# Optimization experiments

Hardware: AMD Instinct MI355X
Metric: run time of the kernel (lower is better)

## Reference

```python
import jax, jax.numpy as jnp
import numpy as np

NHEAD = 8
NEG_INF = -1e9
LN_EPS = 1e-5


def setup_inputs() -> dict:
    key = jax.random.key(0)
    ks = jax.random.split(key, 8)
    B, Q, N, C = 2, 256, 16384, 256
    return {
        "queries": jax.random.normal(ks[0], (B, Q, C), jnp.float32),
        "vid_features": jax.random.normal(ks[1], (B, C, N), jnp.float32),
        "vid_mask": jax.random.uniform(ks[2], (B, Q, N), jnp.float32),
        "pos_embed": jax.random.normal(ks[3], (B, C, N), jnp.float32),
        "query_embed": jax.random.normal(ks[4], (B, Q, C), jnp.float32),
        "in_proj_w": jax.random.normal(ks[5], (3 * C, C), jnp.float32) * 0.02,
        "in_proj_b": jnp.zeros((3 * C,), jnp.float32),
        "out_proj_w": jax.random.normal(ks[6], (C, C), jnp.float32) * 0.02,
        "out_proj_b": jnp.zeros((C,), jnp.float32),
        "ln_gamma": jnp.ones((C,), jnp.float32),
        "ln_beta": jnp.zeros((C,), jnp.float32),
    }


def reference(queries, vid_features, vid_mask, pos_embed, query_embed,
              in_proj_w, in_proj_b, out_proj_w, out_proj_b, ln_gamma, ln_beta):
    B, Q, C = queries.shape
    H = NHEAD
    d = C // H

    vf = jnp.transpose(vid_features, (0, 2, 1))   # B N C
    pe = jnp.transpose(pos_embed, (0, 2, 1))      # B N C

    q_in = queries + query_embed                  # with_pos_embed on queries
    k_in = vf + pe                                # with_pos_embed on keys
    v_in = vf

    wq, wk, wv = jnp.split(in_proj_w, 3, axis=0)
    bq, bk, bv = jnp.split(in_proj_b, 3)

    q = (q_in @ wq.T + bq).reshape(B, Q, H, d)
    k = (k_in @ wk.T + bk).reshape(B, -1, H, d)
    v = (v_in @ wv.T + bv).reshape(B, -1, H, d)

    scale = 1.0 / jnp.sqrt(jnp.asarray(d, q.dtype))
    logits = jnp.einsum('bqhd,bnhd->bhqn', q, k) * scale  # B H Q N

    # Hard masking: block keys where mask prob < 0.5; if a query row is
    # fully blocked, fall back to unmasked attention (avoid NaN softmax).
    blocked = vid_mask < 0.5                                 # B Q N
    all_blocked = jnp.all(blocked, axis=-1, keepdims=True)   # B Q 1
    blocked = blocked & jnp.logical_not(all_blocked)
    logits = jnp.where(blocked[:, None, :, :], NEG_INF, logits)

    attn = jax.nn.softmax(logits, axis=-1)
    ctx = jnp.einsum('bhqn,bnhd->bqhd', attn, v).reshape(B, Q, C)
    tgt2 = ctx @ out_proj_w.T + out_proj_b

    # residual + LayerNorm (dropout p=0.0 -> identity)
    x = queries + tgt2
    mu = jnp.mean(x, axis=-1, keepdims=True)
    var = jnp.mean(jnp.square(x - mu), axis=-1, keepdims=True)
    return (x - mu) / jnp.sqrt(var + LN_EPS) * ln_gamma + ln_beta
```

## Files before the change

kernel.cpp:

```cpp
#include <hip/hip_runtime.h>
#include <stdint.h>

#define B_ 2
#define Q_ 256
#define N_ 16384
#define C_ 256
#define H_ 8
#define D_ 32
#define NC_ 32
#define SCALE 0.17677669529663687f

typedef __bf16 bf16x8 __attribute__((ext_vector_type(8)));
typedef float f32x4 __attribute__((ext_vector_type(4)));

__device__ __forceinline__ uint16_t f2bf(float f) {
  union { float f; uint32_t u; } c; c.f = f;
  uint32_t r = c.u + 0x7FFFu + ((c.u >> 16) & 1u);
  return (uint16_t)(r >> 16);
}
__device__ __forceinline__ float bf2f(uint16_t u) {
  union { uint32_t u; float f; } c; c.u = (uint32_t)u << 16;
  return c.f;
}
__device__ __forceinline__ uint32_t pk2(float a, float b) {
  return (uint32_t)f2bf(a) | ((uint32_t)f2bf(b) << 16);
}
__device__ __forceinline__ void lgkm0_barrier() {
  __builtin_amdgcn_sched_barrier(0);
  asm volatile("s_waitcnt lgkmcnt(0)" ::: "memory");
  __builtin_amdgcn_sched_barrier(0);
  __builtin_amdgcn_s_barrier();
  __builtin_amdgcn_sched_barrier(0);
}

__global__ __launch_bounds__(256) void prep(const float* __restrict__ inw,
                                            const float* __restrict__ outw,
                                            const float* __restrict__ vm,
                                            uint16_t* __restrict__ wb,
                                            float* __restrict__ woT,
                                            uint32_t* __restrict__ mb) {
  __shared__ __align__(16) char sh[4352];
  const int bid = blockIdx.x;
  const int t = threadIdx.x;
  if (bid < 96) {
    const int i = (bid * 256 + t) * 8;
    const float4 a = *reinterpret_cast<const float4*>(inw + i);
    const float4 b = *reinterpret_cast<const float4*>(inw + i + 4);
    ushort4 lo = {f2bf(a.x), f2bf(a.y), f2bf(a.z), f2bf(a.w)};
    ushort4 hi = {f2bf(b.x), f2bf(b.y), f2bf(b.z), f2bf(b.w)};
    *reinterpret_cast<ushort4*>(wb + i) = lo;
    *reinterpret_cast<ushort4*>(wb + i + 4) = hi;
  } else if (bid < 160) {
    float(*s)[33] = reinterpret_cast<float(*)[33]>(sh);
    const int bb = bid - 96;
    const int bx = bb & 7, by = bb >> 3;
    const int r0 = by * 32, c0 = bx * 32;
    const int tr = t >> 5, tc = t & 31;
#pragma unroll
    for (int k = 0; k < 4; ++k)
      s[tr + 8 * k][tc] = outw[(size_t)(r0 + tr + 8 * k) * 256 + c0 + tc];
    __syncthreads();
#pragma unroll
    for (int k = 0; k < 4; ++k)
      woT[(size_t)(c0 + tr + 8 * k) * 256 + r0 + tc] = s[tc][tr + 8 * k];
  } else {
    uint8_t(*nib)[256] = reinterpret_cast<uint8_t(*)[256]>(sh);
    __shared__ int wcnt[4];
    __shared__ int tot;
    const int bq = bid - 160;
    const float* row = vm + (size_t)bq * N_;
    const int lane = t & 63;
    int cnt = 0;
#pragma unroll
    for (int i = 0; i < 16; ++i) {
      const float4 v = *reinterpret_cast<const float4*>(&row[i * 1024 + 4 * t]);
      const uint32_t nb = (v.x < 0.5f ? 1u : 0u) | (v.y < 0.5f ? 2u : 0u) |
                          (v.z < 0.5f ? 4u : 0u) | (v.w < 0.5f ? 8u : 0u);
      nib[i][t] = (uint8_t)nb;
      cnt += __popc(nb);
    }
    for (int o = 32; o > 0; o >>= 1) cnt += __shfl_down(cnt, o, 64);
    if (lane == 0) wcnt[t >> 6] = cnt;
    __syncthreads();
    if (t == 0) tot = wcnt[0] + wcnt[1] + wcnt[2] + wcnt[3];
    __syncthreads();
    const bool allb = (tot == N_);
    uint32_t* dst = mb + (size_t)bq * 512;
#pragma unroll
    for (int k = 0; k < 2; ++k) {
      const int w = k * 256 + t;
      const int i = w >> 5, tw = w & 31;
      const uint2 u = *reinterpret_cast<const uint2*>(&nib[i][8 * tw]);
      uint32_t y0 = u.x & 0x0F0F0F0Fu; y0 = y0 | (y0 >> 4);
      uint32_t y1 = u.y & 0x0F0F0F0Fu; y1 = y1 | (y1 >> 4);
      const uint32_t word = (y0 & 0xFFu) | (((y0 >> 16) & 0xFFu) << 8) |
                            ((y1 & 0xFFu) << 16) | (((y1 >> 16) & 0xFFu) << 24);
      dst[w] = allb ? 0u : word;
    }
  }
}

__global__ __launch_bounds__(512, 2) void kvqproj(const float* __restrict__ vf,
                                                  const float* __restrict__ pe,
                                                  const float* __restrict__ queries,
                                                  const float* __restrict__ qembed,
                                                  const uint16_t* __restrict__ wkv,
                                                  const float* __restrict__ bias,
                                                  uint16_t* __restrict__ Kh,
                                                  uint16_t* __restrict__ Vh,
                                                  uint16_t* __restrict__ Qb) {
  __shared__ __align__(16) uint16_t shpool[8][64][40];
  const int bid = blockIdx.x;
  const int t = threadIdx.x, wid = t >> 6, lane = t & 63;
  const int g = lane >> 4, c15 = lane & 15;

  if (bid >= 8) {
    const int kb = bid - 8;
    const bool isK = kb < 512;
    const int u = isK ? kb : kb - 512;
    const int b = u >> 8, nt = u & 255;
    const int n0 = nt * 64;
    const int wc = wid;

    const uint16_t* Wsec = wkv + (size_t)((isK ? 256 : 512) + wc * 32 + c15) * C_;

    f32x4 acc[8];
    if (isK) {
#pragma unroll
      for (int cf = 0; cf < 2; ++cf) {
        f32x4 iv;
#pragma unroll
        for (int j = 0; j < 4; ++j) iv[j] = bias[256 + wc * 32 + cf * 16 + 4 * g + j];
#pragma unroll
        for (int nf = 0; nf < 4; ++nf) acc[cf * 4 + nf] = iv;
      }
    } else {
#pragma unroll
      for (int cf = 0; cf < 2; ++cf) {
        const float bv = bias[512 + wc * 32 + cf * 16 + c15];
        const f32x4 iv = {bv, bv, bv, bv};
#pragma unroll
        for (int nf = 0; nf < 4; ++nf) acc[nf * 2 + cf] = iv;
      }
    }

    const int cq = t >> 5, q2 = t & 31;
    const float* Xb = vf + ((size_t)b * C_ + 2 * cq) * N_ + n0 + 2 * q2;
    const float* Pb = pe + ((size_t)b * C_ + 2 * cq) * N_ + n0 + 2 * q2;
    const int cqs = cq ^ (((q2 >> 2) & 3) << 2);

    float2 xA0, xA1, pA0, pA1, xB0, xB1, pB0, pB1;
    bf16x8 Wa[2], Wz[2];

#define LOADW(W, s)                                                          \
    {                                                                        \
      _Pragma("unroll") for (int cf = 0; cf < 2; ++cf)                       \
          W[cf] = *(const bf16x8*)(Wsec + (size_t)cf * 16 * C_ + (s) * 32 + g * 8); \
    }
#define LOADA(X0, X1, P0, P1, s)                                             \
    {                                                                        \
      const float* x_ = Xb + (size_t)(s) * 32 * N_;                          \
      X0 = *(const float2*)x_;                                               \
      X1 = *(const float2*)(x_ + N_);                                        \
      if (isK) {                                                             \
        const float* p_ = Pb + (size_t)(s) * 32 * N_;                        \
        P0 = *(const float2*)p_;                                             \
        P1 = *(const float2*)(p_ + N_);                                      \
      }                                                                      \
    }
#define WRITEA(X0, X1, P0, P1, buf)                                          \
    {                                                                        \
      uint32_t w0_, w1_;                                                     \
      if (isK) {                                                             \
        w0_ = pk2(X0.x + P0.x, X1.x + P1.x);                                 \
        w1_ = pk2(X0.y + P0.y, X1.y + P1.y);                                 \
      } else {                                                               \
        w0_ = pk2(X0.x, X1.x);                                               \
        w1_ = pk2(X0.y, X1.y);                                               \
      }                                                                      \
      *(uint32_t*)&shpool[buf][2 * q2][2 * cqs] = w0_;                       \
      *(uint32_t*)&shpool[buf][2 * q2 + 1][2 * cqs] = w1_;                   \
    }
#define COMPUTE(buf, W)                                                      \
    {                                                                        \
      _Pragma("unroll") for (int nf = 0; nf < 4; ++nf) {                     \
        const int r_ = nf * 16 + c15;                                        \
        const bf16x8 F_ = *(const bf16x8*)&shpool[buf][r_][(g ^ ((r_ >> 3) & 3)) * 8]; \
        if (isK) {                                                           \
          _Pragma("unroll") for (int cf = 0; cf < 2; ++cf)                   \
              acc[cf * 4 + nf] = __builtin_amdgcn_mfma_f32_16x16x32_bf16(    \
                  W[cf], F_, acc[cf * 4 + nf], 0, 0, 0);                     \
        } else {                                                             \
          _Pragma("unroll") for (int cf = 0; cf < 2; ++cf)                   \
              acc[nf * 2 + cf] = __builtin_amdgcn_mfma_f32_16x16x32_bf16(    \
                  F_, W[cf], acc[nf * 2 + cf], 0, 0, 0);                     \
        }                                                                    \
      }                                                                      \
    }

    LOADW(Wa, 0);
    LOADA(xA0, xA1, pA0, pA1, 0);
    LOADA(xB0, xB1, pB0, pB1, 1);
    LOADW(Wz, 1); WRITEA(xA0, xA1, pA0, pA1, 0); LOADA(xA0, xA1, pA0, pA1, 2);
    lgkm0_barrier(); COMPUTE(0, Wa); __builtin_amdgcn_sched_barrier(0);
    LOADW(Wa, 2); WRITEA(xB0, xB1, pB0, pB1, 1); LOADA(xB0, xB1, pB0, pB1, 3);
    lgkm0_barrier(); COMPUTE(1, Wz); __builtin_amdgcn_sched_barrier(0);
    LOADW(Wz, 3); WRITEA(xA0, xA1, pA0, pA1, 0); LOADA(xA0, xA1, pA0, pA1, 4);
    lgkm0_barrier(); COMPUTE(0, Wa); __builtin_amdgcn_sched_barrier(0);
    LOADW(Wa, 4); WRITEA(xB0, xB1, pB0, pB1, 1); LOADA(xB0, xB1, pB0, pB1, 5);
    lgkm0_barrier(); COMPUTE(1, Wz); __builtin_amdgcn_sched_barrier(0);
    LOADW(Wz, 5); WRITEA(xA0, xA1, pA0, pA1, 0); LOADA(xA0, xA1, pA0, pA1, 6);
    lgkm0_barrier(); COMPUTE(0, Wa); __builtin_amdgcn_sched_barrier(0);
    LOADW(Wa, 6); WRITEA(xB0, xB1, pB0, pB1, 1); LOADA(xB0, xB1, pB0, pB1, 7);
    lgkm0_barrier(); COMPUTE(1, Wz); __builtin_amdgcn_sched_barrier(0);
    LOADW(Wz, 7); WRITEA(xA0, xA1, pA0, pA1, 0);
    lgkm0_barrier(); COMPUTE(0, Wa); __builtin_amdgcn_sched_barrier(0);
    WRITEA(xB0, xB1, pB0, pB1, 1);
    lgkm0_barrier(); COMPUTE(1, Wz); __builtin_amdgcn_sched_barrier(0);

#undef LOADW
#undef LOADA
#undef WRITEA
#undef COMPUTE

    if (isK) {
      uint16_t* Kp = Kh + (size_t)(b * H_ + wc) * N_ * D_;
#pragma unroll
      for (int cf = 0; cf < 2; ++cf)
#pragma unroll
        for (int nf = 0; nf < 4; ++nf) {
          const f32x4 a = acc[cf * 4 + nf];
          uint2 pkv;
          pkv.x = pk2(a[0], a[1]);
          pkv.y = pk2(a[2], a[3]);
          *(uint2*)&Kp[(size_t)(n0 + nf * 16 + c15) * D_ + cf * 16 + 4 * g] = pkv;
        }
    } else {
      uint16_t* Vp = Vh + (size_t)(b * H_ + wc) * D_ * N_;
#pragma unroll
      for (int nf = 0; nf < 4; ++nf)
#pragma unroll
        for (int cf = 0; cf < 2; ++cf) {
          const f32x4 a = acc[nf * 2 + cf];
          uint2 pkv;
          pkv.x = pk2(a[0], a[1]);
          pkv.y = pk2(a[2], a[3]);
          *(uint2*)&Vp[(size_t)(cf * 16 + c15) * N_ + n0 + nf * 16 + 4 * g] = pkv;
        }
    }
  } else {
    const int qb = bid;
    const int q0g = qb * 64;
    const int b = q0g >> 8, q0 = q0g & 255;
    const int r = t >> 3, c0 = (t & 7) * 32, s = t & 7;
    const float* Qrow = queries + (size_t)(q0g + r) * C_ + c0;
    const float* Erow = qembed + (size_t)(q0g + r) * C_ + c0;
#pragma unroll
    for (int ph = 0; ph < 2; ++ph) {
      float4 a4[4], e4[4];
#pragma unroll
      for (int k = 0; k < 4; ++k) a4[k] = reinterpret_cast<const float4*>(Qrow + ph * 16)[k];
#pragma unroll
      for (int k = 0; k < 4; ++k) e4[k] = reinterpret_cast<const float4*>(Erow + ph * 16)[k];
      const float* af = reinterpret_cast<const float*>(a4);
      const float* ef = reinterpret_cast<const float*>(e4);
#pragma unroll
      for (int i = 0; i < 16; ++i) {
        const int cl = ph * 16 + i;
        const int col = cl ^ (8 * ((r >> 3) & 3));
        shpool[s][r][col] = f2bf(af[i] + ef[i]);
      }
      __builtin_amdgcn_sched_barrier(0);
    }
    lgkm0_barrier();

    const int w = wid;
    f32x4 acc[4][2];
#pragma unroll
    for (int nf = 0; nf < 2; ++nf) {
      const float bv = bias[w * 32 + nf * 16 + c15];
      const f32x4 iv = {bv, bv, bv, bv};
#pragma unroll
      for (int qf = 0; qf < 4; ++qf) acc[qf][nf] = iv;
    }
#pragma unroll
    for (int s8 = 0; s8 < 8; ++s8) {
      bf16x8 Bf[2];
#pragma unroll
      for (int nf = 0; nf < 2; ++nf)
        Bf[nf] = *reinterpret_cast<const bf16x8*>(
            wkv + (size_t)(w * 32 + nf * 16 + c15) * C_ + s8 * 32 + g * 8);
#pragma unroll
      for (int qf = 0; qf < 4; ++qf) {
        const int rr = qf * 16 + c15;
        const bf16x8 Af = *reinterpret_cast<const bf16x8*>(
            &shpool[s8][rr][8 * (g ^ ((rr >> 3) & 3))]);
#pragma unroll
        for (int nf = 0; nf < 2; ++nf)
          acc[qf][nf] = __builtin_amdgcn_mfma_f32_16x16x32_bf16(Af, Bf[nf], acc[qf][nf], 0, 0, 0);
      }
    }
#pragma unroll
    for (int qf = 0; qf < 4; ++qf)
#pragma unroll
      for (int nf = 0; nf < 2; ++nf)
#pragma unroll
        for (int j = 0; j < 4; ++j) {
          const int q = q0 + qf * 16 + 4 * g + j;
          const int dk = nf * 16 + c15;
          Qb[((size_t)(b * H_ + w) * Q_ + q) * D_ + dk] = f2bf(acc[qf][nf][j] * SCALE);
        }
  }
}

__global__ __launch_bounds__(512) void attn(const uint16_t* __restrict__ Qb,
                                            const uint16_t* __restrict__ Kh,
                                            const uint16_t* __restrict__ Vh,
                                            const uint32_t* __restrict__ mb,
                                            uint16_t* __restrict__ ctx_part,
                                            float* __restrict__ lsum_part) {
  const int bid = blockIdx.x;
  const int nc = bid & 31, h = (bid >> 5) & 7, b = bid >> 8;
  const int t = threadIdx.x, wid = t >> 6, lane = t & 63;
  const int g = lane >> 4, c15 = lane & 15;
  const int qw0 = wid * 32;
  const int nbase = nc * (N_ / NC_);
  constexpr int SS = (N_ / NC_) / 128;

  __shared__ __align__(16) uint16_t kst[2][128][40];
  __shared__ __align__(16) uint16_t vst[2][32][136];
  __shared__ __align__(16) uint16_t plds[8][32][40];

  const uint16_t* Qp = Qb + (size_t)(b * H_ + h) * Q_ * D_;
  bf16x8 qfr[2];
#pragma unroll
  for (int qf = 0; qf < 2; ++qf)
    qfr[qf] = *reinterpret_cast<const bf16x8*>(Qp + (size_t)(qw0 + qf * 16 + c15) * D_ + g * 8);

  f32x4 acc[2][2];
  const f32x4 zero4 = {0.f, 0.f, 0.f, 0.f};
#pragma unroll
  for (int qf = 0; qf < 2; ++qf)
#pragma unroll
    for (int dvf = 0; dvf < 2; ++dvf) acc[qf][dvf] = zero4;
  float lsum[2][4] = {};

  const uint32_t* mrow = mb + (size_t)b * Q_ * (N_ / 32);

  const int krow = t >> 2, kch = t & 3;
  const uint16_t* ksrc = Kh + ((size_t)(b * H_ + h) * N_ + nbase + krow) * 32 + kch * 8;
  const int vrow = t >> 4, vch = t & 15;
  const uint16_t* vsrc = Vh + ((size_t)(b * H_ + h) * 32 + vrow) * N_ + nbase + vch * 8;

  uint4 kreg = *(const uint4*)ksrc;
  uint4 vreg = *(const uint4*)vsrc;

  int cur = 0;
  for (int ss = 0; ss < SS; ++ss) {
    *(uint4*)&kst[cur][krow][kch * 8] = kreg;
    *(uint4*)&vst[cur][vrow][vch * 8] = vreg;
    if (ss < SS - 1) {
      kreg = *(const uint4*)(ksrc + (size_t)(ss + 1) * 128 * 32);
      vreg = *(const uint4*)(vsrc + (ss + 1) * 128);
    }
    lgkm0_barrier();

    const int nstart = nbase + ss * 128;
#pragma unroll
    for (int half = 0; half < 2; ++half) {
      uint32_t mw[2][4][2];
#pragma unroll
      for (int qf = 0; qf < 2; ++qf)
#pragma unroll
        for (int j = 0; j < 4; ++j) {
          const int q = qw0 + qf * 16 + 4 * g + j;
          const uint2 u = *reinterpret_cast<const uint2*>(
              &mrow[(size_t)q * (N_ / 32) + (nstart >> 5) + half * 2]);
          mw[qf][j][0] = u.x;
          mw[qf][j][1] = u.y;
        }
#pragma unroll
      for (int s2 = 0; s2 < 2; ++s2) {
        const int sub = half * 2 + s2;
        const int nl0 = sub * 32;
        bf16x8 kfr[2];
#pragma unroll
        for (int nf = 0; nf < 2; ++nf)
          kfr[nf] = *reinterpret_cast<const bf16x8*>(&kst[cur][nl0 + nf * 16 + c15][g * 8]);
        f32x4 s[2][2];
#pragma unroll
        for (int qf = 0; qf < 2; ++qf)
#pragma unroll
          for (int nf = 0; nf < 2; ++nf)
            s[qf][nf] = __builtin_amdgcn_mfma_f32_16x16x32_bf16(qfr[qf], kfr[nf], zero4, 0, 0, 0);

#pragma unroll
        for (int qf = 0; qf < 2; ++qf) {
#pragma unroll
          for (int j = 0; j < 4; ++j) {
            const uint32_t wmask = mw[qf][j][s2];
#pragma unroll
            for (int nf = 0; nf < 2; ++nf) {
              const int bit = nf * 16 + c15;
              const float p = ((wmask >> bit) & 1u) ? 0.0f : __expf(s[qf][nf][j]);
              lsum[qf][j] += p;
              plds[wid][qf * 16 + 4 * g + j][nf * 16 + c15] = f2bf(p);
            }
          }
        }
        __asm__ volatile("s_waitcnt lgkmcnt(0)" ::: "memory");
#pragma unroll
        for (int qf = 0; qf < 2; ++qf) {
          const bf16x8 pa = *reinterpret_cast<const bf16x8*>(&plds[wid][qf * 16 + c15][g * 8]);
#pragma unroll
          for (int dvf = 0; dvf < 2; ++dvf) {
            const bf16x8 vb =
                *reinterpret_cast<const bf16x8*>(&vst[cur][dvf * 16 + c15][nl0 + g * 8]);
            acc[qf][dvf] = __builtin_amdgcn_mfma_f32_16x16x32_bf16(pa, vb, acc[qf][dvf], 0, 0, 0);
          }
        }
      }
    }
    __builtin_amdgcn_sched_barrier(0);
    cur ^= 1;
  }

#pragma unroll
  for (int qf = 0; qf < 2; ++qf)
#pragma unroll
    for (int j = 0; j < 4; ++j) {
      float v = lsum[qf][j];
      v += __shfl_xor(v, 1, 64);
      v += __shfl_xor(v, 2, 64);
      v += __shfl_xor(v, 4, 64);
      v += __shfl_xor(v, 8, 64);
      lsum[qf][j] = v;
    }

  uint16_t* cp = ctx_part + ((size_t)(b * H_ + h) * NC_ + nc) * Q_ * D_;
#pragma unroll
  for (int qf = 0; qf < 2; ++qf)
#pragma unroll
    for (int dvf = 0; dvf < 2; ++dvf)
#pragma unroll
      for (int j = 0; j < 4; ++j) {
        const int q = qw0 + qf * 16 + 4 * g + j;
        cp[(size_t)q * D_ + dvf * 16 + c15] = f2bf(acc[qf][dvf][j]);
      }
  if (c15 == 0) {
    float* lp = lsum_part + ((size_t)(b * H_ + h) * NC_ + nc) * Q_;
#pragma unroll
    for (int qf = 0; qf < 2; ++qf)
#pragma unroll
      for (int j = 0; j < 4; ++j) lp[qw0 + qf * 16 + 4 * g + j] = lsum[qf][j];
  }
}

__global__ __launch_bounds__(256) void epilogue(const uint16_t* __restrict__ ctx_part,
                                                const float* __restrict__ lsum_part,
                                                const float* __restrict__ queries,
                                                const float* __restrict__ woT,
                                                const float* __restrict__ bo,
                                                const float* __restrict__ gamma,
                                                const float* __restrict__ beta,
                                                float* __restrict__ out) {
  const int bq = blockIdx.x;
  const int b = bq >> 8, q = bq & 255;
  const int t = threadIdx.x;
  const int h = t >> 5, dv = t & 31;
  float cs = 0.f, ls = 0.f;
#pragma unroll 8
  for (int k = 0; k < NC_; ++k) {
    cs += bf2f(ctx_part[(((size_t)(b * H_ + h) * NC_ + k) * Q_ + q) * D_ + dv]);
    ls += lsum_part[((size_t)(b * H_ + h) * NC_ + k) * Q_ + q];
  }
  __shared__ float ctxrow[C_];
  ctxrow[t] = cs / ls;
  __syncthreads();
  float acc = bo[t];
#pragma unroll 8
  for (int j = 0; j < C_; ++j) acc = fmaf(ctxrow[j], woT[(size_t)j * C_ + t], acc);
  const float x = queries[(size_t)bq * C_ + t] + acc;
  float s1 = x, s2 = x * x;
  for (int o = 32; o > 0; o >>= 1) {
    s1 += __shfl_down(s1, o, 64);
    s2 += __shfl_down(s2, o, 64);
  }
  __shared__ float r1[4], r2[4];
  if ((t & 63) == 0) { r1[t >> 6] = s1; r2[t >> 6] = s2; }
  __syncthreads();
  const float mu = (r1[0] + r1[1] + r1[2] + r1[3]) * (1.0f / C_);
  const float e2 = (r2[0] + r2[1] + r2[2] + r2[3]) * (1.0f / C_);
  const float var = e2 - mu * mu;
  out[(size_t)bq * C_ + t] = (x - mu) * rsqrtf(var + 1e-5f) * gamma[t] + beta[t];
}

extern "C" void kernel_launch(void* const* d_in, const int* in_sizes, int n_in,
                              void* d_out, int out_size, void* d_ws, size_t ws_size,
                              hipStream_t stream) {
  const float* queries    = (const float*)d_in[0];
  const float* vidfeat    = (const float*)d_in[1];
  const float* vidmask    = (const float*)d_in[2];
  const float* posembed   = (const float*)d_in[3];
  const float* queryembed = (const float*)d_in[4];
  const float* inw        = (const float*)d_in[5];
  const float* inb        = (const float*)d_in[6];
  const float* outw       = (const float*)d_in[7];
  const float* outb       = (const float*)d_in[8];
  const float* gamma      = (const float*)d_in[9];
  const float* beta       = (const float*)d_in[10];
  float* out = (float*)d_out;

  char* ws = (char*)d_ws;
  size_t off = 0;
  uint16_t* Qb   = (uint16_t*)(ws + off); off += (size_t)B_ * H_ * Q_ * D_ * 2;
  uint16_t* Kh   = (uint16_t*)(ws + off); off += (size_t)B_ * H_ * N_ * D_ * 2;
  uint16_t* Vh   = (uint16_t*)(ws + off); off += (size_t)B_ * H_ * D_ * N_ * 2;
  uint32_t* mb   = (uint32_t*)(ws + off); off += (size_t)B_ * Q_ * (N_ / 32) * 4;
  uint16_t* wkv  = (uint16_t*)(ws + off); off += (size_t)768 * C_ * 2;
  float* woT     = (float*)(ws + off);    off += (size_t)C_ * C_ * 4;
  uint16_t* ctxp = (uint16_t*)(ws + off); off += (size_t)B_ * H_ * NC_ * Q_ * D_ * 2;
  float* lsump   = (float*)(ws + off);    off += (size_t)B_ * H_ * NC_ * Q_ * 4;

  prep<<<dim3(672), dim3(256), 0, stream>>>(inw, outw, vidmask, wkv, woT, mb);
  kvqproj<<<dim3(1032), dim3(512), 0, stream>>>(vidfeat, posembed, queries, queryembed,
                                                wkv, inb, Kh, Vh, Qb);
  attn<<<dim3(B_ * H_ * NC_), dim3(512), 0, stream>>>(Qb, Kh, Vh, mb, ctxp, lsump);
  epilogue<<<dim3(B_ * Q_), dim3(256), 0, stream>>>(ctxp, lsump, queries, woT, outb,
                                                    gamma, beta, out);
}
```

Baseline: 104.2 us.

## Fuse K and V projections into one block sharing vid_features tile loads

Each kvqproj block now computes both the K and V projections for its 64-key tile, so vid_features is read from global memory once rather than twice. The grid shrinks from 1032 to 520 blocks and the LDS buffers hold both the pos-embedded and raw tiles. Float-to-bf16 conversion also switches from a manual rounding routine to the compiler's __bf16 cast, which may lower to hardware conversion instructions. The cost is doubled accumulator registers per thread and fewer blocks, which may reduce occupancy and latency hiding.

```diff
diff --git a/kernel.cpp b/kernel.cpp
--- a/kernel.cpp
+++ b/kernel.cpp
@@ -13,17 +13,17 @@
 typedef __bf16 bf16x8 __attribute__((ext_vector_type(8)));
 typedef float f32x4 __attribute__((ext_vector_type(4)));
 
-__device__ __forceinline__ uint16_t f2bf(float f) {
-  union { float f; uint32_t u; } c; c.f = f;
-  uint32_t r = c.u + 0x7FFFu + ((c.u >> 16) & 1u);
-  return (uint16_t)(r >> 16);
+__device__ __forceinline__ uint16_t bfbits(float f) {
+  union { __bf16 h; uint16_t u; } c; c.h = (__bf16)f; return c.u;
 }
 __device__ __forceinline__ float bf2f(uint16_t u) {
   union { uint32_t u; float f; } c; c.u = (uint32_t)u << 16;
   return c.f;
 }
 __device__ __forceinline__ uint32_t pk2(float a, float b) {
-  return (uint32_t)f2bf(a) | ((uint32_t)f2bf(b) << 16);
+  union { struct { uint16_t lo, hi; } s; uint32_t u; } c;
+  c.s.lo = bfbits(a); c.s.hi = bfbits(b);
+  return c.u;
 }
 __device__ __forceinline__ void lgkm0_barrier() {
   __builtin_amdgcn_sched_barrier(0);
@@ -46,8 +46,8 @@
     const int i = (bid * 256 + t) * 8;
     const float4 a = *reinterpret_cast<const float4*>(inw + i);
     const float4 b = *reinterpret_cast<const float4*>(inw + i + 4);
-    ushort4 lo = {f2bf(a.x), f2bf(a.y), f2bf(a.z), f2bf(a.w)};
-    ushort4 hi = {f2bf(b.x), f2bf(b.y), f2bf(b.z), f2bf(b.w)};
+    ushort4 lo = {bfbits(a.x), bfbits(a.y), bfbits(a.z), bfbits(a.w)};
+    ushort4 hi = {bfbits(b.x), bfbits(b.y), bfbits(b.z), bfbits(b.w)};
     *reinterpret_cast<ushort4*>(wb + i) = lo;
     *reinterpret_cast<ushort4*>(wb + i + 4) = hi;
   } else if (bid < 160) {
@@ -116,31 +116,26 @@
 
   if (bid >= 8) {
     const int kb = bid - 8;
-    const bool isK = kb < 512;
-    const int u = isK ? kb : kb - 512;
-    const int b = u >> 8, nt = u & 255;
+    const int b = kb >> 8, nt = kb & 255;
     const int n0 = nt * 64;
-    const int wc = wid;
-
-    const uint16_t* Wsec = wkv + (size_t)((isK ? 256 : 512) + wc * 32 + c15) * C_;
-
-    f32x4 acc[8];
-    if (isK) {
-#pragma unroll
-      for (int cf = 0; cf < 2; ++cf) {
-        f32x4 iv;
-#pragma unroll
-        for (int j = 0; j < 4; ++j) iv[j] = bias[256 + wc * 32 + cf * 16 + 4 * g + j];
-#pragma unroll
-        for (int nf = 0; nf < 4; ++nf) acc[cf * 4 + nf] = iv;
-      }
-    } else {
-#pragma unroll
-      for (int cf = 0; cf < 2; ++cf) {
-        const float bv = bias[512 + wc * 32 + cf * 16 + c15];
-        const f32x4 iv = {bv, bv, bv, bv};
-#pragma unroll
-        for (int nf = 0; nf < 4; ++nf) acc[nf * 2 + cf] = iv;
+    const int w = wid;
+
+    const uint16_t* WsecK = wkv + (size_t)(256 + w * 32 + c15) * C_;
+    const uint16_t* WsecV = wkv + (size_t)(512 + w * 32 + c15) * C_;
+
+    f32x4 acck[8];
+    f32x4 accv[8];
+#pragma unroll
+    for (int cf = 0; cf < 2; ++cf) {
+      f32x4 ivk;
+#pragma unroll
+      for (int j = 0; j < 4; ++j) ivk[j] = bias[256 + w * 32 + cf * 16 + 4 * g + j];
+      const float bv = bias[512 + w * 32 + cf * 16 + c15];
+      const f32x4 ivv = {bv, bv, bv, bv};
+#pragma unroll
+      for (int nf = 0; nf < 4; ++nf) {
+        acck[cf * 4 + nf] = ivk;
+        accv[nf * 2 + cf] = ivv;
       }
     }
 
@@ -150,104 +145,93 @@
     const int cqs = cq ^ (((q2 >> 2) & 3) << 2);
 
     float2 xA0, xA1, pA0, pA1, xB0, xB1, pB0, pB1;
-    bf16x8 Wa[2], Wz[2];
-
-#define LOADW(W, s)                                                          \
+    bf16x8 Wk[2], Wv[2];
+
+#define LOADW(s)                                                             \
     {                                                                        \
-      _Pragma("unroll") for (int cf = 0; cf < 2; ++cf)                       \
-          W[cf] = *(const bf16x8*)(Wsec + (size_t)cf * 16 * C_ + (s) * 32 + g * 8); \
+      _Pragma("unroll") for (int cf = 0; cf < 2; ++cf) {                     \
+        Wk[cf] = *(const bf16x8*)(WsecK + (size_t)cf * 16 * C_ + (s) * 32 + g * 8); \
+        Wv[cf] = *(const bf16x8*)(WsecV + (size_t)cf * 16 * C_ + (s) * 32 + g * 8); \
+      }                                                                      \
     }
 #define LOADA(X0, X1, P0, P1, s)                                             \
     {                                                                        \
       const float* x_ = Xb + (size_t)(s) * 32 * N_;                          \
+      const float* p_ = Pb + (size_t)(s) * 32 * N_;                          \
       X0 = *(const float2*)x_;                                               \
       X1 = *(const float2*)(x_ + N_);                                        \
-      if (isK) {                                                             \
-        const float* p_ = Pb + (size_t)(s) * 32 * N_;                        \
-        P0 = *(const float2*)p_;                                             \
-        P1 = *(const float2*)(p_ + N_);                                      \
-      }                                                                      \
-    }
-#define WRITEA(X0, X1, P0, P1, buf)                                          \
+      P0 = *(const float2*)p_;                                               \
+      P1 = *(const float2*)(p_ + N_);                                        \
+    }
+#define WRITEA(X0, X1, P0, P1, bufp)                                         \
     {                                                                        \
-      uint32_t w0_, w1_;                                                     \
-      if (isK) {                                                             \
-        w0_ = pk2(X0.x + P0.x, X1.x + P1.x);                                 \
-        w1_ = pk2(X0.y + P0.y, X1.y + P1.y);                                 \
-      } else {                                                               \
-        w0_ = pk2(X0.x, X1.x);                                               \
-        w1_ = pk2(X0.y, X1.y);                                               \
-      }                                                                      \
-      *(uint32_t*)&shpool[buf][2 * q2][2 * cqs] = w0_;                       \
-      *(uint32_t*)&shpool[buf][2 * q2 + 1][2 * cqs] = w1_;                   \
-    }
-#define COMPUTE(buf, W)                                                      \
+      *(uint32_t*)&shpool[bufp][2 * q2][2 * cqs]     = pk2(X0.x + P0.x, X1.x + P1.x); \
+      *(uint32_t*)&shpool[bufp][2 * q2 + 1][2 * cqs] = pk2(X0.y + P0.y, X1.y + P1.y); \
+      *(uint32_t*)&shpool[(bufp) + 1][2 * q2][2 * cqs]     = pk2(X0.x, X1.x); \
+      *(uint32_t*)&shpool[(bufp) + 1][2 * q2 + 1][2 * cqs] = pk2(X0.y, X1.y); \
+    }
+#define COMPUTE(bufp)                                                        \
     {                                                                        \
       _Pragma("unroll") for (int nf = 0; nf < 4; ++nf) {                     \
         const int r_ = nf * 16 + c15;                                        \
-        const bf16x8 F_ = *(const bf16x8*)&shpool[buf][r_][(g ^ ((r_ >> 3) & 3)) * 8]; \
-        if (isK) {                                                           \
-          _Pragma("unroll") for (int cf = 0; cf < 2; ++cf)                   \
-              acc[cf * 4 + nf] = __builtin_amdgcn_mfma_f32_16x16x32_bf16(    \
-                  W[cf], F_, acc[cf * 4 + nf], 0, 0, 0);                     \
-        } else {                                                             \
-          _Pragma("unroll") for (int cf = 0; cf < 2; ++cf)                   \
-              acc[nf * 2 + cf] = __builtin_amdgcn_mfma_f32_16x16x32_bf16(    \
-                  F_, W[cf], acc[nf * 2 + cf], 0, 0, 0);                     \
+        const int o_ = (g ^ ((r_ >> 3) & 3)) * 8;                            \
+        const bf16x8 Fp = *(const bf16x8*)&shpool[bufp][r_][o_];             \
+        const bf16x8 Fv = *(const bf16x8*)&shpool[(bufp) + 1][r_][o_];       \
+        _Pragma("unroll") for (int cf = 0; cf < 2; ++cf) {                   \
+          acck[cf * 4 + nf] = __builtin_amdgcn_mfma_f32_16x16x32_bf16(       \
+              Wk[cf], Fp, acck[cf * 4 + nf], 0, 0, 0);                       \
+          accv[nf * 2 + cf] = __builtin_amdgcn_mfma_f32_16x16x32_bf16(       \
+              Fv, Wv[cf], accv[nf * 2 + cf], 0, 0, 0);                       \
         }                                                                    \
       }                                                                      \
     }
 
-    LOADW(Wa, 0);
     LOADA(xA0, xA1, pA0, pA1, 0);
     LOADA(xB0, xB1, pB0, pB1, 1);
-    LOADW(Wz, 1); WRITEA(xA0, xA1, pA0, pA1, 0); LOADA(xA0, xA1, pA0, pA1, 2);
-    lgkm0_barrier(); COMPUTE(0, Wa); __builtin_amdgcn_sched_barrier(0);
-    LOADW(Wa, 2); WRITEA(xB0, xB1, pB0, pB1, 1); LOADA(xB0, xB1, pB0, pB1, 3);
-    lgkm0_barrier(); COMPUTE(1, Wz); __builtin_amdgcn_sched_barrier(0);
-    LOADW(Wz, 3); WRITEA(xA0, xA1, pA0, pA1, 0); LOADA(xA0, xA1, pA0, pA1, 4);
-    lgkm0_barrier(); COMPUTE(0, Wa); __builtin_amdgcn_sched_barrier(0);
-    LOADW(Wa, 4); WRITEA(xB0, xB1, pB0, pB1, 1); LOADA(xB0, xB1, pB0, pB1, 5);
-    lgkm0_barrier(); COMPUTE(1, Wz); __builtin_amdgcn_sched_barrier(0);
-    LOADW(Wz, 5); WRITEA(xA0, xA1, pA0, pA1, 0); LOADA(xA0, xA1, pA0, pA1, 6);
-    lgkm0_barrier(); COMPUTE(0, Wa); __builtin_amdgcn_sched_barrier(0);
-    LOADW(Wa, 6); WRITEA(xB0, xB1, pB0, pB1, 1); LOADA(xB0, xB1, pB0, pB1, 7);
-    lgkm0_barrier(); COMPUTE(1, Wz); __builtin_amdgcn_sched_barrier(0);
-    LOADW(Wz, 7); WRITEA(xA0, xA1, pA0, pA1, 0);
-    lgkm0_barrier(); COMPUTE(0, Wa); __builtin_amdgcn_sched_barrier(0);
-    WRITEA(xB0, xB1, pB0, pB1, 1);
-    lgkm0_barrier(); COMPUTE(1, Wz); __builtin_amdgcn_sched_barrier(0);
+    LOADW(0); WRITEA(xA0, xA1, pA0, pA1, 0); LOADA(xA0, xA1, pA0, pA1, 2);
+    lgkm0_barrier(); COMPUTE(0); __builtin_amdgcn_sched_barrier(0);
+    LOADW(1); WRITEA(xB0, xB1, pB0, pB1, 2); LOADA(xB0, xB1, pB0, pB1, 3);
+    lgkm0_barrier(); COMPUTE(2); __builtin_amdgcn_sched_barrier(0);
+    LOADW(2); WRITEA(xA0, xA1, pA0, pA1, 0); LOADA(xA0, xA1, pA0, pA1, 4);
+    lgkm0_barrier(); COMPUTE(0); __builtin_amdgcn_sched_barrier(0);
+    LOADW(3); WRITEA(xB0, xB1, pB0, pB1, 2); LOADA(xB0, xB1, pB0, pB1, 5);
+    lgkm0_barrier(); COMPUTE(2); __builtin_amdgcn_sched_barrier(0);
+    LOADW(4); WRITEA(xA0, xA1, pA0, pA1, 0); LOADA(xA0, xA1, pA0, pA1, 6);
+    lgkm0_barrier(); COMPUTE(0); __builtin_amdgcn_sched_barrier(0);
+    LOADW(5); WRITEA(xB0, xB1, pB0, pB1, 2); LOADA(xB0, xB1, pB0, pB1, 7);
+    lgkm0_barrier(); COMPUTE(2); __builtin_amdgcn_sched_barrier(0);
+    LOADW(6); WRITEA(xA0, xA1, pA0, pA1, 0);
+    lgkm0_barrier(); COMPUTE(0); __builtin_amdgcn_sched_barrier(0);
+    LOADW(7); WRITEA(xB0, xB1, pB0, pB1, 2);
+    lgkm0_barrier(); COMPUTE(2); __builtin_amdgcn_sched_barrier(0);
 
 #undef LOADW
 #undef LOADA
 #undef WRITEA
 #undef COMPUTE
 
-    if (isK) {
-      uint16_t* Kp = Kh + (size_t)(b * H_ + wc) * N_ * D_;
-#pragma unroll
-      for (int cf = 0; cf < 2; ++cf)
-#pragma unroll
-        for (int nf = 0; nf < 4; ++nf) {
-          const f32x4 a = acc[cf * 4 + nf];
-          uint2 pkv;
-          pkv.x = pk2(a[0], a[1]);
-          pkv.y = pk2(a[2], a[3]);
-          *(uint2*)&Kp[(size_t)(n0 + nf * 16 + c15) * D_ + cf * 16 + 4 * g] = pkv;
-        }
-    } else {
-      uint16_t* Vp = Vh + (size_t)(b * H_ + wc) * D_ * N_;
-#pragma unroll
-      for (int nf = 0; nf < 4; ++nf)
-#pragma unroll
-        for (int cf = 0; cf < 2; ++cf) {
-          const f32x4 a = acc[nf * 2 + cf];
-          uint2 pkv;
-          pkv.x = pk2(a[0], a[1]);
-          pkv.y = pk2(a[2], a[3]);
-          *(uint2*)&Vp[(size_t)(cf * 16 + c15) * N_ + n0 + nf * 16 + 4 * g] = pkv;
-        }
-    }
+    uint16_t* Kp = Kh + (size_t)(b * H_ + w) * N_ * D_;
+#pragma unroll
+    for (int cf = 0; cf < 2; ++cf)
+#pragma unroll
+      for (int nf = 0; nf < 4; ++nf) {
+        const f32x4 a = acck[cf * 4 + nf];
+        uint2 pkv;
+        pkv.x = pk2(a[0], a[1]);
+        pkv.y = pk2(a[2], a[3]);
+        *(uint2*)&Kp[(size_t)(n0 + nf * 16 + c15) * D_ + cf * 16 + 4 * g] = pkv;
+      }
+    uint16_t* Vp = Vh + (size_t)(b * H_ + w) * D_ * N_;
+#pragma unroll
+    for (int nf = 0; nf < 4; ++nf)
+#pragma unroll
+      for (int cf = 0; cf < 2; ++cf) {
+        const f32x4 a = accv[nf * 2 + cf];
+        uint2 pkv;
+        pkv.x = pk2(a[0], a[1]);
+        pkv.y = pk2(a[2], a[3]);
+        *(uint2*)&Vp[(size_t)(cf * 16 + c15) * N_ + n0 + nf * 16 + 4 * g] = pkv;
+      }
   } else {
     const int qb = bid;
     const int q0g = qb * 64;
@@ -268,7 +252,7 @@
       for (int i = 0; i < 16; ++i) {
         const int cl = ph * 16 + i;
         const int col = cl ^ (8 * ((r >> 3) & 3));
-        shpool[s][r][col] = f2bf(af[i] + ef[i]);
+        shpool[s][r][col] = bfbits(af[i] + ef[i]);
       }
       __builtin_amdgcn_sched_barrier(0);
     }
@@ -308,7 +292,7 @@
         for (int j = 0; j < 4; ++j) {
           const int q = q0 + qf * 16 + 4 * g + j;
           const int dk = nf * 16 + c15;
-          Qb[((size_t)(b * H_ + w) * Q_ + q) * D_ + dk] = f2bf(acc[qf][nf][j] * SCALE);
+          Qb[((size_t)(b * H_ + w) * Q_ + q) * D_ + dk] = bfbits(acc[qf][nf][j] * SCALE);
         }
   }
 }
@@ -404,7 +388,7 @@
               const int bit = nf * 16 + c15;
               const float p = ((wmask >> bit) & 1u) ? 0.0f : __expf(s[qf][nf][j]);
               lsum[qf][j] += p;
-              plds[wid][qf * 16 + 4 * g + j][nf * 16 + c15] = f2bf(p);
+              plds[wid][qf * 16 + 4 * g + j][nf * 16 + c15] = bfbits(p);
             }
           }
         }
@@ -445,7 +429,7 @@
 #pragma unroll
       for (int j = 0; j < 4; ++j) {
         const int q = qw0 + qf * 16 + 4 * g + j;
-        cp[(size_t)q * D_ + dvf * 16 + c15] = f2bf(acc[qf][dvf][j]);
+        cp[(size_t)q * D_ + dvf * 16 + c15] = bfbits(acc[qf][dvf][j]);
       }
   if (c15 == 0) {
     float* lp = lsum_part + ((size_t)(b * H_ + h) * NC_ + nc) * Q_;
@@ -523,8 +507,8 @@
   float* lsump   = (float*)(ws + off);    off += (size_t)B_ * H_ * NC_ * Q_ * 4;
 
   prep<<<dim3(672), dim3(256), 0, stream>>>(inw, outw, vidmask, wkv, woT, mb);
-  kvqproj<<<dim3(1032), dim3(512), 0, stream>>>(vidfeat, posembed, queries, queryembed,
-                                                wkv, inb, Kh, Vh, Qb);
+  kvqproj<<<dim3(520), dim3(512), 0, stream>>>(vidfeat, posembed, queries, queryembed,
+                                               wkv, inb, Kh, Vh, Qb);
   attn<<<dim3(B_ * H_ * NC_), dim3(512), 0, stream>>>(Qb, Kh, Vh, mb, ctxp, lsump);
   epilogue<<<dim3(B_ * Q_), dim3(256), 0, stream>>>(ctxp, lsump, queries, woT, outb,
                                                     gamma, beta, out);
```

Result: faster. 95.20 us (-8.7%).
